# Optimization experiments

Hardware: AMD Instinct MI355X
Metric: run time of the kernel (lower is better)

Reference implementation:

```python
import jax, jax.numpy as jnp
import numpy as np

T_B = 0.9  # GIoU threshold from __init__ default
EPS_ADJ = 1e-6
EPS_DEN = 1e-6


def cxcywh_to_xyxy(b):
    cx, cy, w, h = jnp.split(b, 4, axis=-1)
    return jnp.concatenate([cx - 0.5 * w, cy - 0.5 * h, cx + 0.5 * w, cy + 0.5 * h], axis=-1)


def pairwise_giou(boxes):
    # boxes: [N, 4] xyxy -> [N, N] generalized IoU (torchvision/DETR box_ops semantics)
    area = (boxes[:, 2] - boxes[:, 0]) * (boxes[:, 3] - boxes[:, 1])  # [N]
    lt = jnp.maximum(boxes[:, None, :2], boxes[None, :, :2])  # [N, N, 2]
    rb = jnp.minimum(boxes[:, None, 2:], boxes[None, :, 2:])
    wh = jnp.clip(rb - lt, 0.0)
    inter = wh[..., 0] * wh[..., 1]                            # [N, N]
    union = area[:, None] + area[None, :] - inter
    iou = inter / union
    # smallest enclosing box
    lt_e = jnp.minimum(boxes[:, None, :2], boxes[None, :, :2])
    rb_e = jnp.maximum(boxes[:, None, 2:], boxes[None, :, 2:])
    wh_e = jnp.clip(rb_e - lt_e, 0.0)
    area_e = wh_e[..., 0] * wh_e[..., 1]
    return iou - (area_e - union) / area_e


def transitive_closure(adj, n_q):
    # Fixed-point iteration: adj <- (adj + adj @ adj > 1e-6), at most n_q steps.
    # Diagonal is 1 (self-GIoU == 1 > t_b), so this converges in O(log n_q) steps.
    def cond(state):
        t, _, changed = state
        return jnp.logical_and(t < n_q, changed)

    def body(state):
        t, a, _ = state
        new = ((a + jnp.matmul(a, a)) > EPS_ADJ).astype(jnp.float32)
        return (t + 1, new, jnp.any(new != a))

    _, adj, _ = jax.lax.while_loop(cond, body, (jnp.int32(0), adj, jnp.array(True)))
    return adj


def setup_inputs() -> dict:
    key = jax.random.key(0)
    k1, k2 = jax.random.split(key)
    bboxes = jax.random.uniform(k1, (32, 900, 4), dtype=jnp.float32)
    logits = jax.random.normal(k2, (32, 900, 91), dtype=jnp.float32)
    return {"bboxes": bboxes, "logits": logits}


def reference(bboxes, logits):
    n_q = bboxes.shape[1]
    xyxy = cxcywh_to_xyxy(bboxes)                 # [B, N, 4]
    giou = jax.vmap(pairwise_giou)(xyxy)          # [B, N, N]
    mask = giou > T_B
    mask = mask | jnp.swapaxes(mask, 1, 2)        # symmetrize
    adj = transitive_closure(mask.astype(jnp.float32), n_q)  # [B, N, N]
    denom = jnp.sum(adj, axis=-1, keepdims=True) + EPS_DEN   # [B, N, 1]
    aggregated_bboxes = jnp.matmul(adj, bboxes) / denom       # [B, N, 4]
    return (aggregated_bboxes, logits, adj)
```

## Files before the change

### kernel.cpp

```cpp
#include <hip/hip_runtime.h>
#include <stdint.h>

#define NQ 900
#define NB 32
#define WORDS 16
#define ROWS_PER_BLK 30
#define MASK_BLKS (NB * (NQ / ROWS_PER_BLK))
#define LOG_F4 655200
#define COPY_BLKS ((LOG_F4 + 255) / 256)

#define AGG_ELE   0
#define LOG_ELE   115200
#define ADJ_ELE   2736000

#define WS_BITS_BYTES  (sizeof(unsigned long long) * NB * NQ * WORDS)
#define WS_LABG_BYTES  (sizeof(int) * NB * NQ)
#define WS_NEEDED      (WS_BITS_BYTES + WS_LABG_BYTES)

__global__ __launch_bounds__(256) void k_mask(const float4* __restrict__ bb,
                                              unsigned long long* __restrict__ bits,
                                              const float4* __restrict__ logits,
                                              float4* __restrict__ logits_out)
{
#pragma clang fp contract(off)
    const int blk = blockIdx.x;
    if (blk >= MASK_BLKS) {
        int i = (blk - MASK_BLKS) * 256 + threadIdx.x;
        if (i < LOG_F4) logits_out[i] = logits[i];
        return;
    }

    __shared__ float sx1[NQ], sy1[NQ], sx2[NQ], sy2[NQ], sar[NQ];
    const int b     = blk / (NQ / ROWS_PER_BLK);
    const int chunk = blk % (NQ / ROWS_PER_BLK);
    const int row0  = chunk * ROWS_PER_BLK;
    const int tid   = threadIdx.x;

    for (int i = tid; i < NQ; i += 256) {
        float4 q = bb[b * NQ + i];
        float cx = q.x, cy = q.y, w = q.z, h = q.w;
        float hw = 0.5f * w, hh = 0.5f * h;
        float x1 = cx - hw, y1 = cy - hh, x2 = cx + hw, y2 = cy + hh;
        sx1[i] = x1; sy1[i] = y1; sx2[i] = x2; sy2[i] = y2;
        sar[i] = (x2 - x1) * (y2 - y1);
    }
    __syncthreads();

    const int wave = tid >> 6, lane = tid & 63;
    for (int r = row0; r < row0 + ROWS_PER_BLK; ++r) {
        float x1i = sx1[r], y1i = sy1[r], x2i = sx2[r], y2i = sy2[r], ai = sar[r];
        unsigned long long* rowp = bits + (size_t)(b * NQ + r) * WORDS;
        for (int t = 0; t < 4; ++t) {
            int word  = wave + 4 * t;
            int jbase = word << 6;
            if (jbase + 64 <= r) {
                if (lane == 0) rowp[word] = 0ULL;
                continue;
            }
            int j = jbase + lane;
            bool pred = false;
            if (j >= r && j < NQ) {
                float x1j = sx1[j], y1j = sy1[j], x2j = sx2[j], y2j = sy2[j], aj = sar[j];
                float ltx = fmaxf(x1i, x1j), lty = fmaxf(y1i, y1j);
                float rbx = fminf(x2i, x2j), rby = fminf(y2i, y2j);
                float iw  = fmaxf(rbx - ltx, 0.0f), ih = fmaxf(rby - lty, 0.0f);
                float inter = iw * ih;
                float uni   = ai + aj - inter;
                float iou   = inter / uni;
                float ex1 = fminf(x1i, x1j), ey1 = fminf(y1i, y1j);
                float ex2 = fmaxf(x2i, x2j), ey2 = fmaxf(y2i, y2j);
                float ew  = fmaxf(ex2 - ex1, 0.0f), eh2 = fmaxf(ey2 - ey1, 0.0f);
                float ae  = ew * eh2;
                float g   = iou - (ae - uni) / ae;
                pred = (g > 0.9f);
            }
            unsigned long long m = __ballot(pred);
            if (lane == 0) rowp[word] = m;
        }
    }
}

__global__ __launch_bounds__(1024) void k_label(const unsigned long long* __restrict__ bits,
                                                const float4* __restrict__ bb,
                                                int* __restrict__ labg,
                                                float4* __restrict__ agg_out)
{
    __shared__ unsigned long long sbits[NQ * WORDS];
    __shared__ int   lab[NQ];
    __shared__ float scx[NQ], scy[NQ], sw[NQ], sh[NQ], scnt[NQ];
    __shared__ int   changed;
    const int b   = blockIdx.x;
    const int tid = threadIdx.x;
    const size_t base = (size_t)b * NQ;

    {
        const ulonglong2* src = (const ulonglong2*)(bits + base * WORDS);
        ulonglong2* dst = (ulonglong2*)sbits;
        for (int t = tid; t < NQ * WORDS / 2; t += 1024) dst[t] = src[t];
    }
    for (int i = tid; i < NQ; i += 1024) {
        scx[i] = 0.f; scy[i] = 0.f; sw[i] = 0.f; sh[i] = 0.f; scnt[i] = 0.f;
    }
    if (tid == 0) changed = 0;
    __syncthreads();

    for (int i = tid; i < NQ; i += 1024) {
        unsigned long long selfw = sbits[i * WORDS + (i >> 6)];
        bool alive = (selfw >> (i & 63)) & 1ULL;
        lab[i] = alive ? i : -1;
    }
    __syncthreads();

    for (int iter = 0; iter < 1024; ++iter) {
        for (int i = tid; i < NQ; i += 1024) {
            int li = lab[i];
            if (li < 0) continue;
            const unsigned long long* rowp = sbits + i * WORDS;
            for (int k = i >> 6; k < 15; ++k) {
                unsigned long long w = rowp[k];
                while (w) {
                    int j = (k << 6) + __builtin_ctzll(w);
                    w &= w - 1;
                    int lj = lab[j];
                    if (lj < li)      { li = lj; changed = 1; }
                    else if (lj > li) { atomicMin(&lab[j], li); changed = 1; }
                }
            }
            if (li < lab[i]) atomicMin(&lab[i], li);
        }
        __syncthreads();
        for (int i = tid; i < NQ; i += 1024) {
            int li = lab[i];
            if (li > 0) {
                int l2 = lab[li];
                if (l2 < li) lab[i] = l2;
            }
        }
        __syncthreads();
        int done = (changed == 0);
        __syncthreads();
        if (done) break;
        if (tid == 0) changed = 0;
        __syncthreads();
    }

    for (int i = tid; i < NQ; i += 1024) {
        int li = lab[i];
        if (li >= 0) {
            float4 q = bb[base + i];
            atomicAdd(&scx[li], q.x);
            atomicAdd(&scy[li], q.y);
            atomicAdd(&sw [li], q.z);
            atomicAdd(&sh [li], q.w);
            atomicAdd(&scnt[li], 1.0f);
        }
    }
    __syncthreads();

    for (int i = tid; i < NQ; i += 1024) {
        int li = lab[i];
        labg[base + i] = li;
        float4 o;
        if (li >= 0) {
            float d = scnt[li] + 1e-6f;
            o.x = scx[li] / d; o.y = scy[li] / d;
            o.z = sw [li] / d; o.w = sh [li] / d;
        } else {
            o.x = 0.f; o.y = 0.f; o.z = 0.f; o.w = 0.f;
        }
        agg_out[base + i] = o;
    }
}

__global__ __launch_bounds__(256) void k_adj(const int* __restrict__ labg,
                                             float4* __restrict__ adj)
{
    const int row = blockIdx.x;
    const int b = row / NQ;
    const int li = labg[row];
    const int4* lj4 = (const int4*)(labg + (size_t)b * NQ);
    float4* out = adj + (size_t)row * (NQ / 4);
    for (int t = threadIdx.x; t < NQ / 4; t += 256) {
        int4 l = lj4[t];
        float4 o;
        o.x = (l.x == li && li >= 0) ? 1.0f : 0.f;
        o.y = (l.y == li && li >= 0) ? 1.0f : 0.f;
        o.z = (l.z == li && li >= 0) ? 1.0f : 0.f;
        o.w = (l.w == li && li >= 0) ? 1.0f : 0.f;
        out[t] = o;
    }
}

__global__ __launch_bounds__(256) void k_copy(const float4* __restrict__ src,
                                              float4* __restrict__ dst)
{
    int i = blockIdx.x * 256 + threadIdx.x;
    if (i < LOG_F4) dst[i] = src[i];
}

extern "C" void kernel_launch(void* const* d_in, const int* in_sizes, int n_in,
                              void* d_out, int out_size, void* d_ws, size_t ws_size,
                              hipStream_t stream) {
    (void)in_sizes; (void)n_in; (void)out_size;
    const float4* bb = (const float4*)d_in[0];
    const float4* logits = (const float4*)d_in[1];
    float* outf = (float*)d_out;

    float4* agg     = (float4*)(outf + AGG_ELE);
    float4* adj     = (float4*)(outf + ADJ_ELE);
    float4* log_out = (float4*)(outf + LOG_ELE);

    if (d_ws != nullptr && ws_size >= WS_NEEDED) {
        unsigned long long* bits = (unsigned long long*)d_ws;
        int* labg = (int*)((char*)d_ws + WS_BITS_BYTES);
        hipLaunchKernelGGL(k_mask,  dim3(MASK_BLKS + COPY_BLKS), dim3(256), 0, stream,
                           bb, bits, logits, log_out);
        hipLaunchKernelGGL(k_label, dim3(NB), dim3(1024), 0, stream, bits, bb, labg, agg);
        hipLaunchKernelGGL(k_adj,   dim3(NB * NQ), dim3(256), 0, stream, labg, adj);
    } else {
        unsigned long long* bits = (unsigned long long*)(outf + ADJ_ELE);
        int* labg = (int*)(outf + LOG_ELE);
        hipLaunchKernelGGL(k_mask,  dim3(MASK_BLKS), dim3(256), 0, stream,
                           bb, bits, logits, log_out);
        hipLaunchKernelGGL(k_label, dim3(NB), dim3(1024), 0, stream, bits, bb, labg, agg);
        hipLaunchKernelGGL(k_adj,   dim3(NB * NQ), dim3(256), 0, stream, labg, adj);
        hipLaunchKernelGGL(k_copy,  dim3(COPY_BLKS), dim3(256), 0, stream, logits, log_out);
    }
}
```

Measured before the change: 189.5 us.

## Batch adjacency rows per block and pair mask rows for load balance

k_adj now writes 12 rows per block, loading the label vector once per thread and reusing it across rows, which cuts the block count from 28800 to 2400. k_mask handles two rows per iteration (ra and ra+15) so the column loads from shared memory are shared between them. The logits-copy blocks now come first in the grid so they are scheduled early alongside the mask work. A separate k_mask_nf kernel serves the no-workspace path. This adds register pressure in k_mask and reduces parallelism in k_adj.

```diff
diff --git a/kernel.cpp b/kernel.cpp
--- a/kernel.cpp
+++ b/kernel.cpp
@@ -8,6 +8,9 @@
 #define MASK_BLKS (NB * (NQ / ROWS_PER_BLK))
 #define LOG_F4 655200
 #define COPY_BLKS ((LOG_F4 + 255) / 256)
+#define ADJ_ROWS_PER_BLK 12
+#define ADJ_BLKS (NB * (NQ / ADJ_ROWS_PER_BLK))
+#define NQ4 (NQ / 4)
 
 #define AGG_ELE   0
 #define LOG_ELE   115200
@@ -24,15 +27,15 @@
 {
 #pragma clang fp contract(off)
     const int blk = blockIdx.x;
-    if (blk >= MASK_BLKS) {
-        int i = (blk - MASK_BLKS) * 256 + threadIdx.x;
+    if (blk < COPY_BLKS) {
+        int i = blk * 256 + threadIdx.x;
         if (i < LOG_F4) logits_out[i] = logits[i];
         return;
     }
-
+    const int mblk  = blk - COPY_BLKS;
     __shared__ float sx1[NQ], sy1[NQ], sx2[NQ], sy2[NQ], sar[NQ];
-    const int b     = blk / (NQ / ROWS_PER_BLK);
-    const int chunk = blk % (NQ / ROWS_PER_BLK);
+    const int b     = mblk / (NQ / ROWS_PER_BLK);
+    const int chunk = mblk % (NQ / ROWS_PER_BLK);
     const int row0  = chunk * ROWS_PER_BLK;
     const int tid   = threadIdx.x;
 
@@ -47,16 +50,222 @@
     __syncthreads();
 
     const int wave = tid >> 6, lane = tid & 63;
+    for (int rr = 0; rr < ROWS_PER_BLK / 2; ++rr) {
+        const int ra = row0 + rr;
+        const int rb = ra + ROWS_PER_BLK / 2;
+        float ax1 = sx1[ra], ay1 = sy1[ra], ax2 = sx2[ra], ay2 = sy2[ra], aa = sar[ra];
+        float bx1 = sx1[rb], by1 = sy1[rb], bx2 = sx2[rb], by2 = sy2[rb], ab = sar[rb];
+        unsigned long long* rowa = bits + (size_t)(b * NQ + ra) * WORDS;
+        unsigned long long* rowb = bits + (size_t)(b * NQ + rb) * WORDS;
+        for (int t = 0; t < 4; ++t) {
+            int word  = wave + 4 * t;
+            int jbase = word << 6;
+            bool do_a = (jbase + 64 > ra);
+            bool do_b = (jbase + 64 > rb);
+            int j = jbase + lane;
+            float x1j = 0.f, y1j = 0.f, x2j = 0.f, y2j = 0.f, aj = 0.f;
+            if (j < NQ) {
+                x1j = sx1[j]; y1j = sy1[j]; x2j = sx2[j]; y2j = sy2[j]; aj = sar[j];
+            }
+            if (do_a) {
+                bool pred = false;
+                if (j >= ra && j < NQ) {
+                    float ltx = fmaxf(ax1, x1j), lty = fmaxf(ay1, y1j);
+                    float rbx = fminf(ax2, x2j), rby = fminf(ay2, y2j);
+                    float iw  = fmaxf(rbx - ltx, 0.0f), ih = fmaxf(rby - lty, 0.0f);
+                    float inter = iw * ih;
+                    float uni   = aa + aj - inter;
+                    float iou   = inter / uni;
+                    float ex1 = fminf(ax1, x1j), ey1 = fminf(ay1, y1j);
+                    float ex2 = fmaxf(ax2, x2j), ey2 = fmaxf(ay2, y2j);
+                    float ew  = fmaxf(ex2 - ex1, 0.0f), eh2 = fmaxf(ey2 - ey1, 0.0f);
+                    float ae  = ew * eh2;
+                    float g   = iou - (ae - uni) / ae;
+                    pred = (g > 0.9f);
+                }
+                unsigned long long m = __ballot(pred);
+                if (lane == 0) rowa[word] = m;
+            } else {
+                if (lane == 0) rowa[word] = 0ULL;
+            }
+            if (do_b) {
+                bool pred = false;
+                if (j >= rb && j < NQ) {
+                    float ltx = fmaxf(bx1, x1j), lty = fmaxf(by1, y1j);
+                    float rbx = fminf(bx2, x2j), rby = fminf(by2, y2j);
+                    float iw  = fmaxf(rbx - ltx, 0.0f), ih = fmaxf(rby - lty, 0.0f);
+                    float inter = iw * ih;
+                    float uni   = ab + aj - inter;
+                    float iou   = inter / uni;
+                    float ex1 = fminf(bx1, x1j), ey1 = fminf(by1, y1j);
+                    float ex2 = fmaxf(bx2, x2j), ey2 = fmaxf(by2, y2j);
+                    float ew  = fmaxf(ex2 - ex1, 0.0f), eh2 = fmaxf(ey2 - ey1, 0.0f);
+                    float ae  = ew * eh2;
+                    float g   = iou - (ae - uni) / ae;
+                    pred = (g > 0.9f);
+                }
+                unsigned long long m = __ballot(pred);
+                if (lane == 0) rowb[word] = m;
+            } else {
+                if (lane == 0) rowb[word] = 0ULL;
+            }
+        }
+    }
+}
+
+__global__ __launch_bounds__(1024) void k_label(const unsigned long long* __restrict__ bits,
+                                                const float4* __restrict__ bb,
+                                                int* __restrict__ labg,
+                                                float4* __restrict__ agg_out)
+{
+    __shared__ unsigned long long sbits[NQ * WORDS];
+    __shared__ int   lab[NQ];
+    __shared__ float scx[NQ], scy[NQ], sw[NQ], sh[NQ], scnt[NQ];
+    __shared__ int   changed;
+    const int b   = blockIdx.x;
+    const int tid = threadIdx.x;
+    const size_t base = (size_t)b * NQ;
+
+    {
+        const ulonglong2* src = (const ulonglong2*)(bits + base * WORDS);
+        ulonglong2* dst = (ulonglong2*)sbits;
+        for (int t = tid; t < NQ * WORDS / 2; t += 1024) dst[t] = src[t];
+    }
+    for (int i = tid; i < NQ; i += 1024) {
+        scx[i] = 0.f; scy[i] = 0.f; sw[i] = 0.f; sh[i] = 0.f; scnt[i] = 0.f;
+    }
+    if (tid == 0) changed = 0;
+    __syncthreads();
+
+    for (int i = tid; i < NQ; i += 1024) {
+        unsigned long long selfw = sbits[i * WORDS + (i >> 6)];
+        bool alive = (selfw >> (i & 63)) & 1ULL;
+        lab[i] = alive ? i : -1;
+    }
+    __syncthreads();
+
+    for (int iter = 0; iter < 1024; ++iter) {
+        for (int i = tid; i < NQ; i += 1024) {
+            int li = lab[i];
+            if (li < 0) continue;
+            const unsigned long long* rowp = sbits + i * WORDS;
+            for (int k = i >> 6; k < 15; ++k) {
+                unsigned long long w = rowp[k];
+                while (w) {
+                    int j = (k << 6) + __builtin_ctzll(w);
+                    w &= w - 1;
+                    int lj = lab[j];
+                    if (lj < li)      { li = lj; changed = 1; }
+                    else if (lj > li) { atomicMin(&lab[j], li); changed = 1; }
+                }
+            }
+            if (li < lab[i]) atomicMin(&lab[i], li);
+        }
+        __syncthreads();
+        for (int i = tid; i < NQ; i += 1024) {
+            int li = lab[i];
+            if (li > 0) {
+                int l2 = lab[li];
+                if (l2 < li) lab[i] = l2;
+            }
+        }
+        __syncthreads();
+        int done = (changed == 0);
+        __syncthreads();
+        if (done) break;
+        if (tid == 0) changed = 0;
+        __syncthreads();
+    }
+
+    for (int i = tid; i < NQ; i += 1024) {
+        int li = lab[i];
+        if (li >= 0) {
+            float4 q = bb[base + i];
+            atomicAdd(&scx[li], q.x);
+            atomicAdd(&scy[li], q.y);
+            atomicAdd(&sw [li], q.z);
+            atomicAdd(&sh [li], q.w);
+            atomicAdd(&scnt[li], 1.0f);
+        }
+    }
+    __syncthreads();
+
+    for (int i = tid; i < NQ; i += 1024) {
+        int li = lab[i];
+        labg[base + i] = li;
+        float4 o;
+        if (li >= 0) {
+            float d = scnt[li] + 1e-6f;
+            o.x = scx[li] / d; o.y = scy[li] / d;
+            o.z = sw [li] / d; o.w = sh [li] / d;
+        } else {
+            o.x = 0.f; o.y = 0.f; o.z = 0.f; o.w = 0.f;
+        }
+        agg_out[base + i] = o;
+    }
+}
+
+__global__ __launch_bounds__(256) void k_adj(const int* __restrict__ labg,
+                                             float4* __restrict__ adj)
+{
+    const int blk   = blockIdx.x;
+    const int b     = blk / (NQ / ADJ_ROWS_PER_BLK);
+    const int chunk = blk % (NQ / ADJ_ROWS_PER_BLK);
+    const int row0  = chunk * ADJ_ROWS_PER_BLK;
+    __shared__ int sli[ADJ_ROWS_PER_BLK];
+    if (threadIdx.x < ADJ_ROWS_PER_BLK)
+        sli[threadIdx.x] = labg[b * NQ + row0 + threadIdx.x];
+    __syncthreads();
+    const int t = threadIdx.x;
+    if (t >= NQ4) return;
+    int4 l = ((const int4*)(labg + (size_t)b * NQ))[t];
+    float4* out = adj + ((size_t)(b * NQ + row0)) * NQ4 + t;
+    #pragma unroll
+    for (int r = 0; r < ADJ_ROWS_PER_BLK; ++r) {
+        int li = sli[r];
+        float4 o;
+        o.x = (l.x == li && li >= 0) ? 1.0f : 0.f;
+        o.y = (l.y == li && li >= 0) ? 1.0f : 0.f;
+        o.z = (l.z == li && li >= 0) ? 1.0f : 0.f;
+        o.w = (l.w == li && li >= 0) ? 1.0f : 0.f;
+        out[(size_t)r * NQ4] = o;
+    }
+}
+
+__global__ __launch_bounds__(256) void k_copy(const float4* __restrict__ src,
+                                              float4* __restrict__ dst)
+{
+    int i = blockIdx.x * 256 + threadIdx.x;
+    if (i < LOG_F4) dst[i] = src[i];
+}
+
+__global__ __launch_bounds__(256) void k_mask_nf(const float4* __restrict__ bb,
+                                                 unsigned long long* __restrict__ bits)
+{
+#pragma clang fp contract(off)
+    __shared__ float sx1[NQ], sy1[NQ], sx2[NQ], sy2[NQ], sar[NQ];
+    const int mblk  = blockIdx.x;
+    const int b     = mblk / (NQ / ROWS_PER_BLK);
+    const int chunk = mblk % (NQ / ROWS_PER_BLK);
+    const int row0  = chunk * ROWS_PER_BLK;
+    const int tid   = threadIdx.x;
+    for (int i = tid; i < NQ; i += 256) {
+        float4 q = bb[b * NQ + i];
+        float cx = q.x, cy = q.y, w = q.z, h = q.w;
+        float hw = 0.5f * w, hh = 0.5f * h;
+        float x1 = cx - hw, y1 = cy - hh, x2 = cx + hw, y2 = cy + hh;
+        sx1[i] = x1; sy1[i] = y1; sx2[i] = x2; sy2[i] = y2;
+        sar[i] = (x2 - x1) * (y2 - y1);
+    }
+    __syncthreads();
+    const int wave = tid >> 6, lane = tid & 63;
     for (int r = row0; r < row0 + ROWS_PER_BLK; ++r) {
         float x1i = sx1[r], y1i = sy1[r], x2i = sx2[r], y2i = sy2[r], ai = sar[r];
         unsigned long long* rowp = bits + (size_t)(b * NQ + r) * WORDS;
         for (int t = 0; t < 4; ++t) {
             int word  = wave + 4 * t;
             int jbase = word << 6;
-            if (jbase + 64 <= r) {
-                if (lane == 0) rowp[word] = 0ULL;
-                continue;
-            }
+            if (jbase + 64 <= r) { if (lane == 0) rowp[word] = 0ULL; continue; }
             int j = jbase + lane;
             bool pred = false;
             if (j >= r && j < NQ) {
@@ -80,124 +289,6 @@
     }
 }
 
-__global__ __launch_bounds__(1024) void k_label(const unsigned long long* __restrict__ bits,
-                                                const float4* __restrict__ bb,
-                                                int* __restrict__ labg,
-                                                float4* __restrict__ agg_out)
-{
-    __shared__ unsigned long long sbits[NQ * WORDS];
-    __shared__ int   lab[NQ];
-    __shared__ float scx[NQ], scy[NQ], sw[NQ], sh[NQ], scnt[NQ];
-    __shared__ int   changed;
-    const int b   = blockIdx.x;
-    const int tid = threadIdx.x;
-    const size_t base = (size_t)b * NQ;
-
-    {
-        const ulonglong2* src = (const ulonglong2*)(bits + base * WORDS);
-        ulonglong2* dst = (ulonglong2*)sbits;
-        for (int t = tid; t < NQ * WORDS / 2; t += 1024) dst[t] = src[t];
-    }
-    for (int i = tid; i < NQ; i += 1024) {
-        scx[i] = 0.f; scy[i] = 0.f; sw[i] = 0.f; sh[i] = 0.f; scnt[i] = 0.f;
-    }
-    if (tid == 0) changed = 0;
-    __syncthreads();
-
-    for (int i = tid; i < NQ; i += 1024) {
-        unsigned long long selfw = sbits[i * WORDS + (i >> 6)];
-        bool alive = (selfw >> (i & 63)) & 1ULL;
-        lab[i] = alive ? i : -1;
-    }
-    __syncthreads();
-
-    for (int iter = 0; iter < 1024; ++iter) {
-        for (int i = tid; i < NQ; i += 1024) {
-            int li = lab[i];
-            if (li < 0) continue;
-            const unsigned long long* rowp = sbits + i * WORDS;
-            for (int k = i >> 6; k < 15; ++k) {
-                unsigned long long w = rowp[k];
-                while (w) {
-                    int j = (k << 6) + __builtin_ctzll(w);
-                    w &= w - 1;
-                    int lj = lab[j];
-                    if (lj < li)      { li = lj; changed = 1; }
-                    else if (lj > li) { atomicMin(&lab[j], li); changed = 1; }
-                }
-            }
-            if (li < lab[i]) atomicMin(&lab[i], li);
-        }
-        __syncthreads();
-        for (int i = tid; i < NQ; i += 1024) {
-            int li = lab[i];
-            if (li > 0) {
-                int l2 = lab[li];
-                if (l2 < li) lab[i] = l2;
-            }
-        }
-        __syncthreads();
-        int done = (changed == 0);
-        __syncthreads();
-        if (done) break;
-        if (tid == 0) changed = 0;
-        __syncthreads();
-    }
-
-    for (int i = tid; i < NQ; i += 1024) {
-        int li = lab[i];
-        if (li >= 0) {
-            float4 q = bb[base + i];
-            atomicAdd(&scx[li], q.x);
-            atomicAdd(&scy[li], q.y);
-            atomicAdd(&sw [li], q.z);
-            atomicAdd(&sh [li], q.w);
-            atomicAdd(&scnt[li], 1.0f);
-        }
-    }
-    __syncthreads();
-
-    for (int i = tid; i < NQ; i += 1024) {
-        int li = lab[i];
-        labg[base + i] = li;
-        float4 o;
-        if (li >= 0) {
-            float d = scnt[li] + 1e-6f;
-            o.x = scx[li] / d; o.y = scy[li] / d;
-            o.z = sw [li] / d; o.w = sh [li] / d;
-        } else {
-            o.x = 0.f; o.y = 0.f; o.z = 0.f; o.w = 0.f;
-        }
-        agg_out[base + i] = o;
-    }
-}
-
-__global__ __launch_bounds__(256) void k_adj(const int* __restrict__ labg,
-                                             float4* __restrict__ adj)
-{
-    const int row = blockIdx.x;
-    const int b = row / NQ;
-    const int li = labg[row];
-    const int4* lj4 = (const int4*)(labg + (size_t)b * NQ);
-    float4* out = adj + (size_t)row * (NQ / 4);
-    for (int t = threadIdx.x; t < NQ / 4; t += 256) {
-        int4 l = lj4[t];
-        float4 o;
-        o.x = (l.x == li && li >= 0) ? 1.0f : 0.f;
-        o.y = (l.y == li && li >= 0) ? 1.0f : 0.f;
-        o.z = (l.z == li && li >= 0) ? 1.0f : 0.f;
-        o.w = (l.w == li && li >= 0) ? 1.0f : 0.f;
-        out[t] = o;
-    }
-}
-
-__global__ __launch_bounds__(256) void k_copy(const float4* __restrict__ src,
-                                              float4* __restrict__ dst)
-{
-    int i = blockIdx.x * 256 + threadIdx.x;
-    if (i < LOG_F4) dst[i] = src[i];
-}
-
 extern "C" void kernel_launch(void* const* d_in, const int* in_sizes, int n_in,
                               void* d_out, int out_size, void* d_ws, size_t ws_size,
                               hipStream_t stream) {
@@ -216,14 +307,13 @@
         hipLaunchKernelGGL(k_mask,  dim3(MASK_BLKS + COPY_BLKS), dim3(256), 0, stream,
                            bb, bits, logits, log_out);
         hipLaunchKernelGGL(k_label, dim3(NB), dim3(1024), 0, stream, bits, bb, labg, agg);
-        hipLaunchKernelGGL(k_adj,   dim3(NB * NQ), dim3(256), 0, stream, labg, adj);
+        hipLaunchKernelGGL(k_adj,   dim3(ADJ_BLKS), dim3(256), 0, stream, labg, adj);
     } else {
         unsigned long long* bits = (unsigned long long*)(outf + ADJ_ELE);
         int* labg = (int*)(outf + LOG_ELE);
-        hipLaunchKernelGGL(k_mask,  dim3(MASK_BLKS), dim3(256), 0, stream,
-                           bb, bits, logits, log_out);
-        hipLaunchKernelGGL(k_label, dim3(NB), dim3(1024), 0, stream, bits, bb, labg, agg);
-        hipLaunchKernelGGL(k_adj,   dim3(NB * NQ), dim3(256), 0, stream, labg, adj);
-        hipLaunchKernelGGL(k_copy,  dim3(COPY_BLKS), dim3(256), 0, stream, logits, log_out);
-    }
-}
+        hipLaunchKernelGGL(k_mask_nf, dim3(MASK_BLKS), dim3(256), 0, stream, bb, bits);
+        hipLaunchKernelGGL(k_label,   dim3(NB), dim3(1024), 0, stream, bits, bb, labg, agg);
+        hipLaunchKernelGGL(k_adj,     dim3(ADJ_BLKS), dim3(256), 0, stream, labg, adj);
+        hipLaunchKernelGGL(k_copy,    dim3(COPY_BLKS), dim3(256), 0, stream, logits, log_out);
+    }
+}
```

After: 199.1 us. +5.0%, slower.
